# Kernel optimization log

Measured on AMD Instinct MI355X. Metric: run time of the kernel, lower is better.

Reference implementation:

```python
import jax, jax.numpy as jnp
import numpy as np

ALPHA, BETA, THETA = 1.0, 1.0, 10.0
WIN_SIZE = 11
SIGMA = 1.5


def _gauss_window(size, sigma, channel):
    g = np.exp(-((np.arange(size) - size // 2) ** 2) / (2.0 * sigma ** 2))
    g = g / g.sum()
    w2 = np.outer(g, g).astype(np.float32)  # [k, k]
    return jnp.asarray(np.tile(w2[None, None], (channel, 1, 1, 1)))  # [C,1,k,k]


def _dwconv_valid(x, w):
    # x: [B,C,H,W], w: [C,1,k,k]; depthwise conv, no padding (matches F.conv2d padd=0, groups=C)
    return jax.lax.conv_general_dilated(
        x, w, window_strides=(1, 1), padding='VALID',
        feature_group_count=x.shape[1],
        dimension_numbers=('NCHW', 'OIHW', 'NCHW'))


def _ssim_loss(img1, img2, window):
    # val_range heuristic: inputs in [0,1) -> L = 1
    L = 1.0
    C1 = (0.01 * L) ** 2
    C2 = (0.03 * L) ** 2
    mu1 = _dwconv_valid(img1, window)
    mu2 = _dwconv_valid(img2, window)
    mu1_sq = mu1 * mu1
    mu2_sq = mu2 * mu2
    mu1_mu2 = mu1 * mu2
    sigma1_sq = _dwconv_valid(img1 * img1, window) - mu1_sq
    sigma2_sq = _dwconv_valid(img2 * img2, window) - mu2_sq
    sigma12 = _dwconv_valid(img1 * img2, window) - mu1_mu2
    v1 = 2.0 * sigma12 + C2
    v2 = sigma1_sq + sigma2_sq + C2
    ssim_map = (2.0 * mu1_mu2 + C1) * v1 / ((mu1_sq + mu2_sq + C1) * v2)
    return 1.0 - jnp.mean(ssim_map)


_LAP2D = np.array([[1.0, 1.0, 1.0],
                   [1.0, -8.0, 1.0],
                   [1.0, 1.0, 1.0]], dtype=np.float32) / 16.0  # kornia normalized (abs-sum=16)


def _laplacian(x):
    # kornia.filters.laplacian(x, 3): reflect padding, normalized 3x3 laplacian, depthwise
    c = x.shape[1]
    k = jnp.asarray(np.tile(_LAP2D[None, None], (c, 1, 1, 1)))  # [C,1,3,3]
    xp = jnp.pad(x, ((0, 0), (0, 0), (1, 1), (1, 1)), mode='reflect')
    return _dwconv_valid(xp, k)


def setup_inputs() -> dict:
    key = jax.random.key(0)
    ks = jax.random.split(key, 5)
    shape = (32, 1, 512, 512)
    names = ['im_fus', 'im_ir', 'im_vi', 'map_ir', 'map_vi']
    return {n: jax.random.uniform(k, shape, dtype=jnp.float32) for n, k in zip(names, ks)}


def reference(im_fus, im_ir, im_vi, map_ir, map_vi):
    window = _gauss_window(WIN_SIZE, SIGMA, im_fus.shape[1])
    ms_ssim_loss = _ssim_loss(im_fus, im_ir, window) + _ssim_loss(im_fus, im_vi, window)
    l1_loss = jnp.mean(jnp.abs(jnp.maximum(map_ir, map_vi) - im_fus))
    ir_grad = jnp.abs(_laplacian(im_ir))
    vi_grad = jnp.abs(_laplacian(im_vi))
    fus_grad = jnp.abs(_laplacian(im_fus))
    grad_loss = jnp.mean(jnp.abs(jnp.maximum(ir_grad, vi_grad) - fus_grad))
    return ALPHA * ms_ssim_loss + BETA * l1_loss + THETA * grad_loss
```

## Files before the change

### kernel.cpp

```cpp
#include <hip/hip_runtime.h>
#include <cmath>


typedef float f32x2 __attribute__((ext_vector_type(2)));

struct GaussW { float w[11]; };

#define SSIM_C1 1.0e-4f
#define SSIM_C2 9.0e-4f

__global__ __launch_bounds__(256, 3)
void ssim_kernel(const float* __restrict__ fus, const float* __restrict__ irp,
                 const float* __restrict__ vip, float* __restrict__ part,
                 GaussW gw)
{
    const int b    = blockIdx.z;
    const int r0   = blockIdx.y * 42;
    const int tid  = threadIdx.x;
    const int wv   = tid >> 6;
    const int lane = tid & 63;
    const int c0   = blockIdx.x * 256 + wv * 64;
    const int out_rows = min(42, 502 - r0);
    const int in_rows  = out_rows + 10;

    const size_t ib = (size_t)b * 512 * 512;
    const float* __restrict__ Fp = fus + ib;
    const float* __restrict__ Ip = irp + ib;
    const float* __restrict__ Vp = vip + ib;

    __shared__ f32x2 srow_fi[4][80];
    __shared__ float srow_v [4][80];

    float w6[6];
#pragma unroll
    for (int k = 0; k < 6; ++k) w6[k] = gw.w[k];

    f32x2 acc[11][4];
#pragma unroll
    for (int s = 0; s < 11; ++s)
#pragma unroll
        for (int q = 0; q < 4; ++q) acc[s][q] = (f32x2)(0.f);

    float lssim = 0.f;
    const int  col      = c0 + lane;
    const bool col_ok   = col <= 501;
    const bool extra    = lane < 10;
    const int  col2     = c0 + 64 + lane;
    const bool extra_ok = extra && (col2 < 512);

    float rf, rg, rv, rf2 = 0.f, rg2 = 0.f, rv2 = 0.f;
    {
        const size_t base = (size_t)r0 * 512 + col;
        rf = Fp[base]; rg = Ip[base]; rv = Vp[base];
        if (extra_ok) {
            const size_t b2 = (size_t)r0 * 512 + col2;
            rf2 = Fp[b2]; rg2 = Ip[b2]; rv2 = Vp[b2];
        }
    }

#pragma unroll 1
    for (int rb = 0; rb < 55; rb += 11) {
#pragma unroll
        for (int p = 0; p < 11; ++p) {
            const int r = rb + p;
            if (r < in_rows) {
                srow_fi[wv][lane] = (f32x2){rf, rg};
                srow_v [wv][lane] = rv;
                if (extra) {
                    srow_fi[wv][64 + lane] = (f32x2){rf2, rg2};
                    srow_v [wv][64 + lane] = rv2;
                }
                __builtin_amdgcn_wave_barrier();

                if (r + 1 < in_rows) {
                    const size_t base = (size_t)(r0 + r + 1) * 512 + col;
                    rf = Fp[base]; rg = Ip[base]; rv = Vp[base];
                    if (extra_ok) {
                        const size_t b2 = (size_t)(r0 + r + 1) * 512 + col2;
                        rf2 = Fp[b2]; rg2 = Ip[b2]; rv2 = Vp[b2];
                    }
                }

                f32x2 hfhi = (f32x2)(0.f);
                f32x2 hffii = (f32x2)(0.f);
                f32x2 hfifv = (f32x2)(0.f);
                f32x2 hvvv = (f32x2)(0.f);
#pragma unroll
                for (int k = 0; k < 11; ++k) {
                    const float t = w6[k < 6 ? k : 10 - k];
                    const f32x2 fi = srow_fi[wv][lane + k];
                    const float V  = srow_v [wv][lane + k];
                    const f32x2 t2 = (f32x2){t, t};
                    const f32x2 tfi = t2 * fi;
                    hfhi  = __builtin_elementwise_fma(t2,  fi, hfhi);
                    hffii = __builtin_elementwise_fma(tfi, fi, hffii);
                    hfifv.x = fmaf(tfi.x, fi.y, hfifv.x);
                    hfifv.y = fmaf(tfi.x, V,    hfifv.y);
                    const float tV = t * V;
                    hvvv.x = fmaf(t,  V, hvvv.x);
                    hvvv.y = fmaf(tV, V, hvvv.y);
                }
                __builtin_amdgcn_wave_barrier();

                {
                    const f32x2 w02 = (f32x2){w6[0], w6[0]};
                    acc[p][0] = w02 * hfhi;
                    acc[p][1] = w02 * hffii;
                    acc[p][2] = w02 * hfifv;
                    acc[p][3] = w02 * hvvv;
                }
#pragma unroll
                for (int k = 1; k < 11; ++k) {
                    const int s = (p - k + 11) % 11;
                    const float t = w6[k < 6 ? k : 10 - k];
                    const f32x2 t2 = (f32x2){t, t};
                    acc[s][0] = __builtin_elementwise_fma(t2, hfhi,  acc[s][0]);
                    acc[s][1] = __builtin_elementwise_fma(t2, hffii, acc[s][1]);
                    acc[s][2] = __builtin_elementwise_fma(t2, hfifv, acc[s][2]);
                    acc[s][3] = __builtin_elementwise_fma(t2, hvvv,  acc[s][3]);
                }
                if (r >= 10) {
                    const int s = (p + 1) % 11;
                    const float mu1 = acc[s][0].x, mu2 = acc[s][0].y, mu3 = acc[s][3].x;
                    const float eff = acc[s][1].x, eii = acc[s][1].y, evv = acc[s][3].y;
                    const float efi = acc[s][2].x, efv = acc[s][2].y;
                    const float mu1sq = mu1*mu1, mu2sq = mu2*mu2, mu3sq = mu3*mu3;
                    const float mu12 = mu1*mu2, mu13 = mu1*mu3;
                    const float sf  = eff - mu1sq;
                    const float si  = eii - mu2sq;
                    const float sv  = evv - mu3sq;
                    const float s12 = efi - mu12;
                    const float s13 = efv - mu13;
                    const float n1 = (2.f*mu12 + SSIM_C1) * (2.f*s12 + SSIM_C2);
                    const float d1 = (mu1sq + mu2sq + SSIM_C1) * (sf + si + SSIM_C2);
                    const float n2 = (2.f*mu13 + SSIM_C1) * (2.f*s13 + SSIM_C2);
                    const float d2 = (mu1sq + mu3sq + SSIM_C1) * (sf + sv + SSIM_C2);
                    const float q1 = __builtin_amdgcn_rcpf(d1);
                    const float q2 = __builtin_amdgcn_rcpf(d2);
                    if (col_ok) lssim += fmaf(n1, q1, n2 * q2);
                }
            }
        }
    }

#pragma unroll
    for (int off = 32; off > 0; off >>= 1)
        lssim += __shfl_down(lssim, off);
    __shared__ float red[4];
    if (lane == 0) red[wv] = lssim;
    __syncthreads();
    if (tid == 0) {
        const int blk = blockIdx.x + 2 * (blockIdx.y + 12 * blockIdx.z);
        part[blk] = red[0] + red[1] + red[2] + red[3];
    }
}

__device__ inline float4 lap3x3(const float* __restrict__ rm,
                                const float* __restrict__ rc,
                                const float* __restrict__ rp,
                                int x0, int xl, int xr, float4& center)
{
    float4 a = *(const float4*)(rm + x0);
    float4 b = *(const float4*)(rc + x0);
    float4 c = *(const float4*)(rp + x0);
    const float aL = rm[xl], bL = rc[xl], cL = rp[xl];
    const float aR = rm[xr], bR = rc[xr], cR = rp[xr];
    const float s0 = aL + bL + cL;
    const float s1 = a.x + b.x + c.x;
    const float s2 = a.y + b.y + c.y;
    const float s3 = a.z + b.z + c.z;
    const float s4 = a.w + b.w + c.w;
    const float s5 = aR + bR + cR;
    center = b;
    float4 l;
    l.x = (s0 + s1 + s2 - 9.f*b.x) * 0.0625f;
    l.y = (s1 + s2 + s3 - 9.f*b.y) * 0.0625f;
    l.z = (s2 + s3 + s4 - 9.f*b.z) * 0.0625f;
    l.w = (s3 + s4 + s5 - 9.f*b.w) * 0.0625f;
    return l;
}

__global__ __launch_bounds__(256, 4)
void lapl1_kernel(const float* __restrict__ fus, const float* __restrict__ irp,
                  const float* __restrict__ vip, const float* __restrict__ mir,
                  const float* __restrict__ mvi,
                  float* __restrict__ part_l1, float* __restrict__ part_gr)
{
    const int b   = blockIdx.y;
    const int tid = threadIdx.x;
    const int xq  = tid & 127;
    const int x0  = xq * 4;
    const size_t ib = (size_t)b * 512 * 512;

    const int xl = (x0 == 0)        ? 1   : x0 - 1;
    const int xr = (x0 + 4 == 512)  ? 510 : x0 + 4;

    const float* Fb = fus + ib;
    const float* Ib = irp + ib;
    const float* Vb = vip + ib;

    float l1s = 0.f, grs = 0.f;

#pragma unroll
    for (int it = 0; it < 4; ++it) {
        const int y  = blockIdx.x * 8 + it * 2 + (tid >> 7);
        const int ym = (y == 0)   ? 1   : y - 1;
        const int yp = (y == 511) ? 510 : y + 1;

        float4 cf, ci, cv;
        const float4 lf = lap3x3(Fb + (size_t)ym*512, Fb + (size_t)y*512, Fb + (size_t)yp*512, x0, xl, xr, cf);
        const float4 li = lap3x3(Ib + (size_t)ym*512, Ib + (size_t)y*512, Ib + (size_t)yp*512, x0, xl, xr, ci);
        const float4 lv = lap3x3(Vb + (size_t)ym*512, Vb + (size_t)y*512, Vb + (size_t)yp*512, x0, xl, xr, cv);

        const float4 m1 = *(const float4*)(mir + ib + (size_t)y*512 + x0);
        const float4 m2 = *(const float4*)(mvi + ib + (size_t)y*512 + x0);

        l1s += fabsf(fmaxf(m1.x, m2.x) - cf.x) + fabsf(fmaxf(m1.y, m2.y) - cf.y)
             + fabsf(fmaxf(m1.z, m2.z) - cf.z) + fabsf(fmaxf(m1.w, m2.w) - cf.w);

        grs += fabsf(fmaxf(fabsf(li.x), fabsf(lv.x)) - fabsf(lf.x))
             + fabsf(fmaxf(fabsf(li.y), fabsf(lv.y)) - fabsf(lf.y))
             + fabsf(fmaxf(fabsf(li.z), fabsf(lv.z)) - fabsf(lf.z))
             + fabsf(fmaxf(fabsf(li.w), fabsf(lv.w)) - fabsf(lf.w));
    }

#pragma unroll
    for (int off = 32; off > 0; off >>= 1) {
        l1s += __shfl_down(l1s, off);
        grs += __shfl_down(grs, off);
    }
    __shared__ float red[8];
    if ((tid & 63) == 0) { red[tid >> 6] = l1s; red[4 + (tid >> 6)] = grs; }
    __syncthreads();
    if (tid == 0) {
        const int blk = blockIdx.x + 64 * blockIdx.y;
        part_l1[blk] = red[0] + red[1] + red[2] + red[3];
        part_gr[blk] = red[4] + red[5] + red[6] + red[7];
    }
}

__global__ void final_kernel(const float* __restrict__ ws, float* __restrict__ out)
{
    const int tid = threadIdx.x;
    float s0 = 0.f, s1 = 0.f, s2 = 0.f;
#pragma unroll
    for (int i = tid; i < 768; i += 256) s0 += ws[i];
#pragma unroll
    for (int i = tid; i < 2048; i += 256) {
        s1 += ws[768 + i];
        s2 += ws[2816 + i];
    }
#pragma unroll
    for (int off = 32; off > 0; off >>= 1) {
        s0 += __shfl_down(s0, off);
        s1 += __shfl_down(s1, off);
        s2 += __shfl_down(s2, off);
    }
    __shared__ float red[12];
    if ((tid & 63) == 0) {
        red[tid >> 6] = s0; red[4 + (tid >> 6)] = s1; red[8 + (tid >> 6)] = s2;
    }
    __syncthreads();
    if (tid == 0) {
        const float ssim_sum = red[0] + red[1] + red[2] + red[3];
        const float l1_sum   = red[4] + red[5] + red[6] + red[7];
        const float gr_sum   = red[8] + red[9] + red[10] + red[11];
        const float ms = 2.f - ssim_sum / 8064128.f;
        const float l1 = l1_sum / 8388608.f;
        const float gr = gr_sum / 8388608.f;
        out[0] = ms + l1 + 10.f * gr;
    }
}

extern "C" void kernel_launch(void* const* d_in, const int* in_sizes, int n_in,
                              void* d_out, int out_size, void* d_ws, size_t ws_size,
                              hipStream_t stream)
{
    const float* fus = (const float*)d_in[0];
    const float* irp = (const float*)d_in[1];
    const float* vip = (const float*)d_in[2];
    const float* mir = (const float*)d_in[3];
    const float* mvi = (const float*)d_in[4];
    float* out = (float*)d_out;
    float* ws  = (float*)d_ws;

    GaussW gw;
    double g[11], s = 0.0;
    for (int i = 0; i < 11; ++i) {
        const double d = (double)i - 5.0;
        g[i] = std::exp(-(d * d) / (2.0 * 1.5 * 1.5));
        s += g[i];
    }
    for (int i = 0; i < 11; ++i) gw.w[i] = (float)(g[i] / s);

    ssim_kernel<<<dim3(2, 12, 32), 256, 0, stream>>>(fus, irp, vip, ws, gw);
    lapl1_kernel<<<dim3(64, 32), 256, 0, stream>>>(fus, irp, vip, mir, mvi,
                                                   ws + 768, ws + 2816);
    final_kernel<<<1, 256, 0, stream>>>(ws, out);
}
```

Baseline: 110.9 us.

## Fuse Laplacian gradient and L1 terms into the SSIM streaming kernel

Computes the 3x3 reflect-padded Laplacian and the L1 term inside the row-streaming SSIM kernel, reusing the image rows already staged in LDS. A left halo column is added, and running column sums form the vertical stencil. This removes the separate lapl1 kernel launch and its second read of the three images. In exchange the SSIM kernel gets more registers (occupancy hint lowered from 3 to 2 blocks per SM) and extra per-row work, and only the 768 SSIM blocks now cover the Laplacian pass.

Measured after the change: 96.47 us. -13.0%, faster.

```diff
diff --git a/kernel.cpp b/kernel.cpp
--- a/kernel.cpp
+++ b/kernel.cpp
@@ -9,24 +9,30 @@
 #define SSIM_C1 1.0e-4f
 #define SSIM_C2 9.0e-4f
 
-__global__ __launch_bounds__(256, 3)
+__global__ __launch_bounds__(256, 2)
 void ssim_kernel(const float* __restrict__ fus, const float* __restrict__ irp,
-                 const float* __restrict__ vip, float* __restrict__ part,
+                 const float* __restrict__ vip, const float* __restrict__ mir,
+                 const float* __restrict__ mvi, float* __restrict__ ws,
                  GaussW gw)
 {
     const int b    = blockIdx.z;
-    const int r0   = blockIdx.y * 42;
+    const int rs   = blockIdx.y;
+    const int r0   = rs * 42;
     const int tid  = threadIdx.x;
     const int wv   = tid >> 6;
     const int lane = tid & 63;
     const int c0   = blockIdx.x * 256 + wv * 64;
     const int out_rows = min(42, 502 - r0);
     const int in_rows  = out_rows + 10;
+    const bool first = (rs == 0);
+    const bool last  = (rs == 11);
 
     const size_t ib = (size_t)b * 512 * 512;
     const float* __restrict__ Fp = fus + ib;
     const float* __restrict__ Ip = irp + ib;
     const float* __restrict__ Vp = vip + ib;
+    mir += ib;
+    mvi += ib;
 
     __shared__ f32x2 srow_fi[4][80];
     __shared__ float srow_v [4][80];
@@ -41,20 +47,28 @@
 #pragma unroll
         for (int q = 0; q < 4; ++q) acc[s][q] = (f32x2)(0.f);
 
-    float lssim = 0.f;
+    float lssim = 0.f, l1s = 0.f, grs = 0.f;
     const int  col      = c0 + lane;
     const bool col_ok   = col <= 501;
-    const bool extra    = lane < 10;
-    const int  col2     = c0 + 64 + lane;
-    const bool extra_ok = extra && (col2 < 512);
+    const bool is_left  = (lane == 10);
+    const int  colH     = is_left ? (c0 - 1) : (c0 + 64 + lane);
+    const bool halo_ok  = (lane < 10) ? (colH < 512) : (is_left && c0 > 0);
+    const int  hidx     = 64 + lane;
+    const int il       = (lane == 0) ? ((c0 == 0) ? 1 : 74) : (lane - 1);
+    const bool rt_edge = (lane == 63) && (c0 + 64 >= 512);
+
+    f32x2 csFI_1 = (f32x2)(0.f), csFI_2 = (f32x2)(0.f);
+    float csV_1 = 0.f, csV_2 = 0.f;
+    f32x2 cPrevFI = (f32x2)(0.f); float cPrevV = 0.f;
+    float m1r = 0.f, m2r = 0.f;
 
     float rf, rg, rv, rf2 = 0.f, rg2 = 0.f, rv2 = 0.f;
     {
-        const size_t base = (size_t)r0 * 512 + col;
-        rf = Fp[base]; rg = Ip[base]; rv = Vp[base];
-        if (extra_ok) {
-            const size_t b2 = (size_t)r0 * 512 + col2;
-            rf2 = Fp[b2]; rg2 = Ip[b2]; rv2 = Vp[b2];
+        const size_t b0 = (size_t)r0 * 512 + col;
+        rf = Fp[b0]; rg = Ip[b0]; rv = Vp[b0];
+        if (halo_ok) {
+            const size_t bh = (size_t)r0 * 512 + colH;
+            rf2 = Fp[bh]; rg2 = Ip[bh]; rv2 = Vp[bh];
         }
     }
 
@@ -64,32 +78,35 @@
         for (int p = 0; p < 11; ++p) {
             const int r = rb + p;
             if (r < in_rows) {
+                const float curF = rf, curI = rg, curV = rv;
                 srow_fi[wv][lane] = (f32x2){rf, rg};
                 srow_v [wv][lane] = rv;
-                if (extra) {
-                    srow_fi[wv][64 + lane] = (f32x2){rf2, rg2};
-                    srow_v [wv][64 + lane] = rv2;
+                if (halo_ok) {
+                    srow_fi[wv][hidx] = (f32x2){rf2, rg2};
+                    srow_v [wv][hidx] = rv2;
                 }
                 __builtin_amdgcn_wave_barrier();
 
                 if (r + 1 < in_rows) {
                     const size_t base = (size_t)(r0 + r + 1) * 512 + col;
                     rf = Fp[base]; rg = Ip[base]; rv = Vp[base];
-                    if (extra_ok) {
-                        const size_t b2 = (size_t)(r0 + r + 1) * 512 + col2;
-                        rf2 = Fp[b2]; rg2 = Ip[b2]; rv2 = Vp[b2];
+                    if (halo_ok) {
+                        const size_t bh = (size_t)(r0 + r + 1) * 512 + colH;
+                        rf2 = Fp[bh]; rg2 = Ip[bh]; rv2 = Vp[bh];
                     }
                 }
 
-                f32x2 hfhi = (f32x2)(0.f);
+                f32x2 hfhi  = (f32x2)(0.f);
                 f32x2 hffii = (f32x2)(0.f);
                 f32x2 hfifv = (f32x2)(0.f);
-                f32x2 hvvv = (f32x2)(0.f);
+                f32x2 hvvv  = (f32x2)(0.f);
+                f32x2 fi1 = (f32x2)(0.f); float v1 = 0.f;
 #pragma unroll
                 for (int k = 0; k < 11; ++k) {
                     const float t = w6[k < 6 ? k : 10 - k];
                     const f32x2 fi = srow_fi[wv][lane + k];
                     const float V  = srow_v [wv][lane + k];
+                    if (k == 1) { fi1 = fi; v1 = V; }
                     const f32x2 t2 = (f32x2){t, t};
                     const f32x2 tfi = t2 * fi;
                     hfhi  = __builtin_elementwise_fma(t2,  fi, hfhi);
@@ -99,6 +116,17 @@
                     const float tV = t * V;
                     hvvv.x = fmaf(t,  V, hvvv.x);
                     hvvv.y = fmaf(tV, V, hvvv.y);
+                }
+
+                const bool lap_row = (r <= 43) || last;
+                f32x2 csFI_cur = (f32x2)(0.f); float csV_cur = 0.f;
+                if (lap_row) {
+                    const f32x2 fiL = srow_fi[wv][il];
+                    const float vL  = srow_v [wv][il];
+                    f32x2 fiR = fi1; float vR = v1;
+                    if (rt_edge) { fiR = fiL; vR = vL; }
+                    csFI_cur = fiL + fiR + (f32x2){curF, curI};
+                    csV_cur  = vL  + vR  + curV;
                 }
                 __builtin_amdgcn_wave_barrier();
 
@@ -139,103 +167,61 @@
                     const float q2 = __builtin_amdgcn_rcpf(d2);
                     if (col_ok) lssim += fmaf(n1, q1, n2 * q2);
                 }
+                if (r >= 2 && lap_row) {
+                    const f32x2 sFI = csFI_2 + csFI_1 + csFI_cur;
+                    const float sV  = csV_2 + csV_1 + csV_cur;
+                    const f32x2 lFI = __builtin_elementwise_fma(
+                                         (f32x2){-9.f,-9.f}, cPrevFI, sFI);
+                    const float lV  = fmaf(-9.f, cPrevV, sV);
+                    grs += fabsf(fmaxf(fabsf(lFI.y), fabsf(lV)) - fabsf(lFI.x));
+                    l1s += fabsf(fmaxf(m1r, m2r) - cPrevFI.x);
+                }
+                if (first && r == 1) {
+                    const f32x2 sFI = csFI_1 + csFI_cur + csFI_cur;
+                    const float sV  = csV_1 + csV_cur + csV_cur;
+                    const f32x2 lFI = __builtin_elementwise_fma(
+                                         (f32x2){-9.f,-9.f}, cPrevFI, sFI);
+                    const float lV  = fmaf(-9.f, cPrevV, sV);
+                    grs += fabsf(fmaxf(fabsf(lFI.y), fabsf(lV)) - fabsf(lFI.x));
+                    l1s += fabsf(fmaxf(m1r, m2r) - cPrevFI.x);
+                }
+                if (lap_row) {
+                    csFI_2 = csFI_1; csFI_1 = csFI_cur;
+                    csV_2  = csV_1;  csV_1  = csV_cur;
+                    cPrevFI = (f32x2){curF, curI}; cPrevV = curV;
+                    const int ny = min(r0 + r, 511);
+                    const size_t bm = (size_t)ny * 512 + col;
+                    m1r = mir[bm]; m2r = mvi[bm];
+                }
             }
         }
     }
 
-#pragma unroll
-    for (int off = 32; off > 0; off >>= 1)
+    if (last) {
+        const size_t bm = (size_t)511 * 512 + col;
+        const float m1e = mir[bm], m2e = mvi[bm];
+        const f32x2 sFI = csFI_2 + csFI_2 + csFI_1;
+        const float sV  = csV_2 + csV_2 + csV_1;
+        const f32x2 lFI = __builtin_elementwise_fma((f32x2){-9.f,-9.f}, cPrevFI, sFI);
+        const float lV  = fmaf(-9.f, cPrevV, sV);
+        grs += fabsf(fmaxf(fabsf(lFI.y), fabsf(lV)) - fabsf(lFI.x));
+        l1s += fabsf(fmaxf(m1e, m2e) - cPrevFI.x);
+    }
+
+#pragma unroll
+    for (int off = 32; off > 0; off >>= 1) {
         lssim += __shfl_down(lssim, off);
-    __shared__ float red[4];
-    if (lane == 0) red[wv] = lssim;
+        l1s   += __shfl_down(l1s, off);
+        grs   += __shfl_down(grs, off);
+    }
+    __shared__ float red[12];
+    if (lane == 0) { red[wv] = lssim; red[4 + wv] = l1s; red[8 + wv] = grs; }
     __syncthreads();
     if (tid == 0) {
         const int blk = blockIdx.x + 2 * (blockIdx.y + 12 * blockIdx.z);
-        part[blk] = red[0] + red[1] + red[2] + red[3];
-    }
-}
-
-__device__ inline float4 lap3x3(const float* __restrict__ rm,
-                                const float* __restrict__ rc,
-                                const float* __restrict__ rp,
-                                int x0, int xl, int xr, float4& center)
-{
-    float4 a = *(const float4*)(rm + x0);
-    float4 b = *(const float4*)(rc + x0);
-    float4 c = *(const float4*)(rp + x0);
-    const float aL = rm[xl], bL = rc[xl], cL = rp[xl];
-    const float aR = rm[xr], bR = rc[xr], cR = rp[xr];
-    const float s0 = aL + bL + cL;
-    const float s1 = a.x + b.x + c.x;
-    const float s2 = a.y + b.y + c.y;
-    const float s3 = a.z + b.z + c.z;
-    const float s4 = a.w + b.w + c.w;
-    const float s5 = aR + bR + cR;
-    center = b;
-    float4 l;
-    l.x = (s0 + s1 + s2 - 9.f*b.x) * 0.0625f;
-    l.y = (s1 + s2 + s3 - 9.f*b.y) * 0.0625f;
-    l.z = (s2 + s3 + s4 - 9.f*b.z) * 0.0625f;
-    l.w = (s3 + s4 + s5 - 9.f*b.w) * 0.0625f;
-    return l;
-}
-
-__global__ __launch_bounds__(256, 4)
-void lapl1_kernel(const float* __restrict__ fus, const float* __restrict__ irp,
-                  const float* __restrict__ vip, const float* __restrict__ mir,
-                  const float* __restrict__ mvi,
-                  float* __restrict__ part_l1, float* __restrict__ part_gr)
-{
-    const int b   = blockIdx.y;
-    const int tid = threadIdx.x;
-    const int xq  = tid & 127;
-    const int x0  = xq * 4;
-    const size_t ib = (size_t)b * 512 * 512;
-
-    const int xl = (x0 == 0)        ? 1   : x0 - 1;
-    const int xr = (x0 + 4 == 512)  ? 510 : x0 + 4;
-
-    const float* Fb = fus + ib;
-    const float* Ib = irp + ib;
-    const float* Vb = vip + ib;
-
-    float l1s = 0.f, grs = 0.f;
-
-#pragma unroll
-    for (int it = 0; it < 4; ++it) {
-        const int y  = blockIdx.x * 8 + it * 2 + (tid >> 7);
-        const int ym = (y == 0)   ? 1   : y - 1;
-        const int yp = (y == 511) ? 510 : y + 1;
-
-        float4 cf, ci, cv;
-        const float4 lf = lap3x3(Fb + (size_t)ym*512, Fb + (size_t)y*512, Fb + (size_t)yp*512, x0, xl, xr, cf);
-        const float4 li = lap3x3(Ib + (size_t)ym*512, Ib + (size_t)y*512, Ib + (size_t)yp*512, x0, xl, xr, ci);
-        const float4 lv = lap3x3(Vb + (size_t)ym*512, Vb + (size_t)y*512, Vb + (size_t)yp*512, x0, xl, xr, cv);
-
-        const float4 m1 = *(const float4*)(mir + ib + (size_t)y*512 + x0);
-        const float4 m2 = *(const float4*)(mvi + ib + (size_t)y*512 + x0);
-
-        l1s += fabsf(fmaxf(m1.x, m2.x) - cf.x) + fabsf(fmaxf(m1.y, m2.y) - cf.y)
-             + fabsf(fmaxf(m1.z, m2.z) - cf.z) + fabsf(fmaxf(m1.w, m2.w) - cf.w);
-
-        grs += fabsf(fmaxf(fabsf(li.x), fabsf(lv.x)) - fabsf(lf.x))
-             + fabsf(fmaxf(fabsf(li.y), fabsf(lv.y)) - fabsf(lf.y))
-             + fabsf(fmaxf(fabsf(li.z), fabsf(lv.z)) - fabsf(lf.z))
-             + fabsf(fmaxf(fabsf(li.w), fabsf(lv.w)) - fabsf(lf.w));
-    }
-
-#pragma unroll
-    for (int off = 32; off > 0; off >>= 1) {
-        l1s += __shfl_down(l1s, off);
-        grs += __shfl_down(grs, off);
-    }
-    __shared__ float red[8];
-    if ((tid & 63) == 0) { red[tid >> 6] = l1s; red[4 + (tid >> 6)] = grs; }
-    __syncthreads();
-    if (tid == 0) {
-        const int blk = blockIdx.x + 64 * blockIdx.y;
-        part_l1[blk] = red[0] + red[1] + red[2] + red[3];
-        part_gr[blk] = red[4] + red[5] + red[6] + red[7];
+        ws[blk]        = red[0] + red[1] + red[2] + red[3];
+        ws[768 + blk]  = red[4] + red[5] + red[6] + red[7];
+        ws[1536 + blk] = (red[8] + red[9] + red[10] + red[11]) * 0.0625f;
     }
 }
 
@@ -244,11 +230,10 @@
     const int tid = threadIdx.x;
     float s0 = 0.f, s1 = 0.f, s2 = 0.f;
 #pragma unroll
-    for (int i = tid; i < 768; i += 256) s0 += ws[i];
-#pragma unroll
-    for (int i = tid; i < 2048; i += 256) {
+    for (int i = tid; i < 768; i += 256) {
+        s0 += ws[i];
         s1 += ws[768 + i];
-        s2 += ws[2816 + i];
+        s2 += ws[1536 + i];
     }
 #pragma unroll
     for (int off = 32; off > 0; off >>= 1) {
@@ -293,8 +278,7 @@
     }
     for (int i = 0; i < 11; ++i) gw.w[i] = (float)(g[i] / s);
 
-    ssim_kernel<<<dim3(2, 12, 32), 256, 0, stream>>>(fus, irp, vip, ws, gw);
-    lapl1_kernel<<<dim3(64, 32), 256, 0, stream>>>(fus, irp, vip, mir, mvi,
-                                                   ws + 768, ws + 2816);
+    ssim_kernel<<<dim3(2, 12, 32), 256, 0, stream>>>(fus, irp, vip, mir, mvi,
+                                                     ws, gw);
     final_kernel<<<1, 256, 0, stream>>>(ws, out);
 }
```
